# Performance work log

Measured on AMD Instinct MI355X. Metric: run time of the kernel, lower is better.

## Reference

```python
import jax, jax.numpy as jnp
import numpy as np

N_HEAD = 16
NEG = -1e30  # finite stand-in for -inf; keeps softmax NaN-free


def setup_inputs() -> dict:
    key = jax.random.key(0)
    k1, k2, k3, k4, k5, k6 = jax.random.split(key, 6)
    B, T, C = 4, 2048, 1024
    x = jax.random.normal(k1, (B, T, C), dtype=jnp.float32)
    # realistic right-padding: True = padded position
    lengths = jax.random.randint(k2, (B,), T // 2, T + 1)  # at least half valid
    padding_mask = jnp.arange(T)[None, :] >= lengths[:, None]  # [B,T] bool
    s = 0.02
    W_attn = jax.random.normal(k3, (C, 3 * C), dtype=jnp.float32) * s
    b_attn = jnp.zeros((3 * C,), dtype=jnp.float32)
    W_proj = jax.random.normal(k4, (C, C), dtype=jnp.float32) * s
    b_proj = jnp.zeros((C,), dtype=jnp.float32)
    return {"x": x, "padding_mask": padding_mask, "W_attn": W_attn,
            "b_attn": b_attn, "W_proj": W_proj, "b_proj": b_proj}


def reference(x, padding_mask, W_attn, b_attn, W_proj, b_proj):
    B, T, C = x.shape
    H, D = N_HEAD, C // N_HEAD
    qkv = x @ W_attn + b_attn  # [B,T,3C]
    q, k, v = jnp.split(qkv, 3, axis=-1)
    q = q.reshape(B, T, H, D).transpose(0, 2, 1, 3)  # [B,H,T,D]
    k = k.reshape(B, T, H, D).transpose(0, 2, 1, 3)
    v = v.reshape(B, T, H, D).transpose(0, 2, 1, 3)
    att = jnp.einsum('bhqd,bhkd->bhqk', q, k) / jnp.sqrt(jnp.float32(D))
    causal = jnp.tril(jnp.ones((T, T), dtype=bool))  # [T,T]
    invalid = padding_mask[:, None, None, :] | ~causal[None, None]  # [B,1,T,T] key invalid
    att = jnp.where(invalid, NEG, att)
    att = jax.nn.softmax(att, axis=-1)
    # rows where every key is masked: torch softmax gives NaN -> nan_to_num(0)
    any_valid = jnp.any(~invalid, axis=-1, keepdims=True)  # [B,1,T,1]
    att = jnp.where(any_valid, att, 0.0)
    y = jnp.einsum('bhqk,bhkd->bhqd', att, v)  # [B,H,T,D]
    y = y.transpose(0, 2, 1, 3).reshape(B, T, C)
    y = y @ W_proj + b_proj
    y = jnp.where(padding_mask[:, :, None], 0.0, y)
    return y
```

## Files before the change

kernel.cpp:

```cpp
#include <hip/hip_runtime.h>
#include <stdint.h>

#define T_SEQ 2048
#define CDIM  1024
#define NH    16
#define DH    64
#define BATCH 4
#define MROWS (BATCH * T_SEQ)
#define N3    (3 * CDIM)
#define NEGBIG -1e30f

typedef unsigned short u16;
typedef __attribute__((ext_vector_type(8))) __bf16 bf16x8;
typedef __attribute__((ext_vector_type(4))) __bf16 bf16x4;
typedef __attribute__((ext_vector_type(8))) unsigned short u16x8;
typedef __attribute__((ext_vector_type(4))) float f32x4;
typedef __attribute__((ext_vector_type(16))) float f32x16;
typedef __attribute__((ext_vector_type(4))) unsigned int u32x4;

__device__ inline u16 f2bf(float f) {
  uint32_t u = __builtin_bit_cast(uint32_t, f);
  u += 0x7FFFu + ((u >> 16) & 1u);
  return (u16)(u >> 16);
}

__device__ inline void gld_lds16(const void* g, void* l) {
  __builtin_amdgcn_global_load_lds(
      (const __attribute__((address_space(1))) void*)g,
      (__attribute__((address_space(3))) void*)l, 16, 0, 0);
}


__global__ __launch_bounds__(256) void cvt_f32_bf16(
    const float* __restrict__ in, u16* __restrict__ out, int n) {
  int i = (blockIdx.x * 256 + threadIdx.x) * 4;
  if (i >= n) return;
  float4 v = *(const float4*)&in[i];
  ushort4 o; o.x = f2bf(v.x); o.y = f2bf(v.y); o.z = f2bf(v.z); o.w = f2bf(v.w);
  *(ushort4*)&out[i] = o;
}

__global__ __launch_bounds__(256) void wt_tiled(
    const float* __restrict__ W, u16* __restrict__ WT, int K, int N) {
  __shared__ float tile[64][65];
  const int k0 = blockIdx.y * 64, n0 = blockIdx.x * 64;
  const int t = threadIdx.x, cr = t >> 6, cc = t & 63;
#pragma unroll
  for (int i = 0; i < 16; i++) {
    int r = i * 4 + cr;
    tile[r][cc] = W[(size_t)(k0 + r) * N + n0 + cc];
  }
  __syncthreads();
#pragma unroll
  for (int i = 0; i < 16; i++) {
    int r = i * 4 + cr;
    WT[(size_t)(n0 + r) * K + k0 + cc] = f2bf(tile[cc][r]);
  }
}

__global__ __launch_bounds__(256) void len_kernel(
    const void* __restrict__ maskp, int* __restrict__ lengths) {
  __shared__ int flag;
  __shared__ int red[256];
  const int t = threadIdx.x, b = blockIdx.x;
  if (t == 0) flag = 0;
  __syncthreads();
  const uint32_t* mw = (const uint32_t*)maskp;
  int f = 0;
  for (int i = t; i < 2048; i += 256) f |= (mw[i] > 1u) ? 1 : 0;
  if (f) atomicOr(&flag, 1);
  __syncthreads();
  int cnt = 0;
  if (flag) {
    const uint8_t* mb = (const uint8_t*)maskp;
    for (int i = t; i < T_SEQ; i += 256) cnt += (mb[(size_t)b * T_SEQ + i] == 0);
  } else {
    const int* mi = (const int*)maskp;
    for (int i = t; i < T_SEQ; i += 256) cnt += (mi[(size_t)b * T_SEQ + i] == 0);
  }
  red[t] = cnt;
  __syncthreads();
  for (int s = 128; s > 0; s >>= 1) {
    if (t < s) red[t] += red[t + s];
    __syncthreads();
  }
  if (t == 0) lengths[b] = red[0];
}

template <int MODE>
__global__ __launch_bounds__(256, 2) void gemm_bf16(
    const u16* __restrict__ A, const u16* __restrict__ Bt,
    const float* __restrict__ bias,
    u16* __restrict__ Qb, u16* __restrict__ Kb, u16* __restrict__ Vt,
    float* __restrict__ Out, const int* __restrict__ lengths,
    int Mdim, int Ndim, int Kdim) {
  __shared__ u16 SM[16384];
  u16* As = SM;
  u16* Bs = SM + 8192;
  const int t = threadIdx.x;
  const int lane = t & 63, wid = t >> 6;
  const int wr = wid >> 1, wc = wid & 1;
  const int r16 = lane & 15, kg = lane >> 4;
  const int m0 = blockIdx.y * 128, n0 = blockIdx.x * 128;

  f32x4 acc[4][4];
#pragma unroll
  for (int i = 0; i < 4; i++)
#pragma unroll
    for (int j = 0; j < 4; j++) acc[i][j] = (f32x4){0.f, 0.f, 0.f, 0.f};

  for (int k0 = 0; k0 < Kdim; k0 += 64) {
#pragma unroll
    for (int i = 0; i < 4; i++) {
      int idx = i * 256 + t;
      int row = idx >> 3;
      int chunk = idx & 7;
      int colel = (chunk * 8) ^ ((row & 7) << 3);
      gld_lds16(&A[(size_t)(m0 + row) * Kdim + k0 + colel], &As[idx * 8]);
      gld_lds16(&Bt[(size_t)(n0 + row) * Kdim + k0 + colel], &Bs[idx * 8]);
    }
    __syncthreads();

#pragma unroll
    for (int s = 0; s < 2; s++) {
      bf16x8 af[4], bfr[4];
#pragma unroll
      for (int m = 0; m < 4; m++) {
        int row = wr * 64 + m * 16 + r16;
        int colel = (s * 32 + kg * 8) ^ ((row & 7) << 3);
        af[m] = *(const bf16x8*)&As[row * 64 + colel];
      }
#pragma unroll
      for (int n = 0; n < 4; n++) {
        int row = wc * 64 + n * 16 + r16;
        int colel = (s * 32 + kg * 8) ^ ((row & 7) << 3);
        bfr[n] = *(const bf16x8*)&Bs[row * 64 + colel];
      }
#pragma unroll
      for (int m = 0; m < 4; m++)
#pragma unroll
        for (int n = 0; n < 4; n++)
          acc[m][n] = __builtin_amdgcn_mfma_f32_16x16x32_bf16(
              af[m], bfr[n], acc[m][n], 0, 0, 0);
    }
    __syncthreads();
  }

  if (MODE == 0 && n0 >= 2048) {
    u16* Tt = SM;
#pragma unroll
    for (int m = 0; m < 4; m++)
#pragma unroll
      for (int n = 0; n < 4; n++) {
        int ln = wc * 64 + n * 16 + r16;
        float bv = bias[n0 + ln];
#pragma unroll
        for (int reg = 0; reg < 4; reg++) {
          int lm = wr * 64 + m * 16 + kg * 4 + reg;
          Tt[ln * 128 + (lm ^ ((ln & 7) << 3))] = f2bf(acc[m][n][reg] + bv);
        }
      }
    __syncthreads();
    const int b = m0 >> 11;
    const int tt0 = m0 & 2047;
    const int cbase = n0 - 2048;
#pragma unroll
    for (int i = 0; i < 8; i++) {
      int u = i * 256 + t;
      int ln = u >> 4, ch = u & 15;
      u16x8 v = *(const u16x8*)&Tt[ln * 128 + ((ch * 8) ^ ((ln & 7) << 3))];
      int c = cbase + ln, hh = c >> 6, d = c & 63;
      *(u16x8*)&Vt[(((size_t)b * NH + hh) * DH + d) * T_SEQ + tt0 + ch * 8] = v;
    }
    return;
  }

#pragma unroll
  for (int m = 0; m < 4; m++) {
    int gmb = m0 + wr * 64 + m * 16 + kg * 4;
#pragma unroll
    for (int n = 0; n < 4; n++) {
      int gn = n0 + wc * 64 + n * 16 + r16;
      float bv = bias[gn];
#pragma unroll
      for (int reg = 0; reg < 4; reg++) {
        float v = acc[m][n][reg] + bv;
        int row = gmb + reg;
        int b = row >> 11, tt = row & 2047;
        if (MODE == 0) {
          int c = gn & 1023, h = c >> 6, d = c & 63;
          u16* dst = (gn < 1024) ? Qb : Kb;
          dst[((size_t)(b * NH + h) * T_SEQ + tt) * DH + d] = f2bf(v);
        } else {
          if (tt >= lengths[b]) v = 0.f;
          Out[(size_t)row * CDIM + gn] = v;
        }
      }
    }
  }
}

__global__ __launch_bounds__(256) void attn32p_kernel(
    const u16* __restrict__ Qb, const u16* __restrict__ Kb,
    const u16* __restrict__ Vt, u16* __restrict__ yb,
    const int* __restrict__ lengths) {
  __shared__ __attribute__((aligned(16))) char smem[32768];
  const int t = threadIdx.x, lane = t & 63, wid = t >> 6;
  const int l31 = lane & 31, hi = lane >> 5;
  const int wgid = blockIdx.x;
  const int xcd = wgid & 7, slot = wgid >> 3;
  const int bh = xcd * 8 + (slot >> 4);
  const int iq = slot & 15;
  const int b = bh >> 4, h = bh & (NH - 1);
  const int len = lengths[b];
  const int n64 = (len + 63) >> 6;
  const int npairs = (n64 + 1) >> 1;
  if (iq >= npairs) return;
  const int q0L = iq * 64;
  const int q0H = (n64 - 1 - iq) * 64;
  const bool hiAct = q0H > q0L;
  const int wp = wid >> 1, w2 = wid & 1;
  const bool act = (wp == 0) || hiAct;
  const int q0w = (wp ? q0H : q0L) + w2 * 32;
  const int qrow = q0w + l31;
  const u16* Qh = Qb + (size_t)bh * T_SEQ * DH;
  const u16* Kh = Kb + (size_t)bh * T_SEQ * DH;
  const u16* Vth = Vt + (size_t)bh * DH * T_SEQ;
  const float SC = 0.18033688011112042f;
  const float THR = 44.3614195558365f;

  const int kv_end = (hiAct ? q0H : q0L) + 64;
  const int ntiles = kv_end >> 6;

  bf16x8 qf[4];
#pragma unroll
  for (int ks = 0; ks < 4; ks++)
    qf[ks] = *(const bf16x8*)&Qh[(size_t)qrow * DH + ks * 16 + hi * 8];

  f32x16 oacc[2];
  oacc[0] = (f32x16)0.f; oacc[1] = (f32x16)0.f;
  float mrun = NEGBIG, lrun = 0.f;

  const int idx0 = t, idx1 = 256 + t;
  const int row0 = idx0 >> 3, ch0 = idx0 & 7;
  const int row1 = idx1 >> 3, ch1 = idx1 & 7;
  const int kc0 = (ch0 * 8) ^ ((row0 & 7) << 3);
  const int kc1 = (ch1 * 8) ^ ((row1 & 7) << 3);
  const char* kp0 = (const char*)Kh + ((size_t)row0 * DH + kc0) * 2;
  const char* kp1 = (const char*)Kh + ((size_t)row1 * DH + kc1) * 2;
  const char* vp0 = (const char*)Vth + ((size_t)row0 * T_SEQ + kc0) * 2;
  const char* vp1 = (const char*)Vth + ((size_t)row1 * T_SEQ + kc1) * 2;

  auto STAGE = [&](int bsel) {
    char* base = smem + bsel * 16384;
    gld_lds16(kp0, base + idx0 * 16);
    gld_lds16(kp1, base + idx1 * 16);
    gld_lds16(vp0, base + 8192 + idx0 * 16);
    gld_lds16(vp1, base + 8192 + idx1 * 16);
    kp0 += 8192; kp1 += 8192; vp0 += 128; vp1 += 128;
  };

  auto FLASH = [&](const u16* Ks, const u16* Vts, int kv0) {
    f32x16 sacc[2];
    sacc[0] = (f32x16)0.f; sacc[1] = (f32x16)0.f;
    __builtin_amdgcn_s_setprio(1);
#pragma unroll
    for (int kb = 0; kb < 2; kb++)
#pragma unroll
      for (int ks = 0; ks < 4; ks++) {
        int row = kb * 32 + l31;
        int col = (ks * 16 + hi * 8) ^ ((row & 7) << 3);
        bf16x8 ak = *(const bf16x8*)&Ks[row * 64 + col];
        sacc[kb] = __builtin_amdgcn_mfma_f32_32x32x16_bf16(
            ak, qf[ks], sacc[kb], 0, 0, 0);
      }
    __builtin_amdgcn_s_setprio(0);

    if ((kv0 + 63 > q0w) || (kv0 + 64 > len)) {
#pragma unroll
      for (int kb = 0; kb < 2; kb++)
#pragma unroll
        for (int r = 0; r < 16; r++) {
          int key = kv0 + kb * 32 + (r & 3) + 8 * (r >> 2) + 4 * hi;
          if (key > qrow || key >= len) sacc[kb][r] = NEGBIG;
        }
    }
    float tm[16];
#pragma unroll
    for (int r = 0; r < 16; r++) tm[r] = fmaxf(sacc[0][r], sacc[1][r]);
#pragma unroll
    for (int r = 0; r < 8; r++) tm[r] = fmaxf(tm[r], tm[r + 8]);
#pragma unroll
    for (int r = 0; r < 4; r++) tm[r] = fmaxf(tm[r], tm[r + 4]);
    tm[0] = fmaxf(fmaxf(tm[0], tm[2]), fmaxf(tm[1], tm[3]));
    float mt = fmaxf(tm[0], __shfl_xor(tm[0], 32));

    if (!__all(mt <= mrun + THR)) {
      float mnew = fmaxf(mrun, mt);
      float fac = exp2f((mrun - mnew) * SC);
      mrun = mnew;
      lrun *= fac;
#pragma unroll
      for (int r = 0; r < 16; r++) { oacc[0][r] *= fac; oacc[1][r] *= fac; }
    }
    const float msc = mrun * SC;
#pragma unroll
    for (int kb = 0; kb < 2; kb++)
#pragma unroll
      for (int r = 0; r < 16; r++)
        sacc[kb][r] = exp2f(fmaf(sacc[kb][r], SC, -msc));
    float pt[16];
#pragma unroll
    for (int r = 0; r < 16; r++) pt[r] = sacc[0][r] + sacc[1][r];
#pragma unroll
    for (int r = 0; r < 8; r++) pt[r] += pt[r + 8];
#pragma unroll
    for (int r = 0; r < 4; r++) pt[r] += pt[r + 4];
    float ps = (pt[0] + pt[2]) + (pt[1] + pt[3]);
    ps += __shfl_xor(ps, 32);
    lrun += ps;

#pragma unroll
    for (int ks = 0; ks < 4; ks++) {
      const int kb = ks >> 1, rb = (ks & 1) * 8;
      uint32_t d0, d1, d2, d3;
      asm("v_cvt_pk_bf16_f32 %0, %1, %2" : "=v"(d0)
          : "v"(sacc[kb][rb + 0]), "v"(sacc[kb][rb + 1]));
      asm("v_cvt_pk_bf16_f32 %0, %1, %2" : "=v"(d1)
          : "v"(sacc[kb][rb + 2]), "v"(sacc[kb][rb + 3]));
      asm("v_cvt_pk_bf16_f32 %0, %1, %2" : "=v"(d2)
          : "v"(sacc[kb][rb + 4]), "v"(sacc[kb][rb + 5]));
      asm("v_cvt_pk_bf16_f32 %0, %1, %2" : "=v"(d3)
          : "v"(sacc[kb][rb + 6]), "v"(sacc[kb][rb + 7]));
      bf16x8 pb = __builtin_bit_cast(bf16x8, (u32x4){d0, d1, d2, d3});
      __builtin_amdgcn_s_setprio(1);
#pragma unroll
      for (int mb = 0; mb < 2; mb++) {
        int row = mb * 32 + l31;
        int sw = (row & 7);
        bf16x4 v1 = *(const bf16x4*)&Vts[row * 64 + ((2 * ks) ^ sw) * 8 + 4 * hi];
        bf16x4 v2 = *(const bf16x4*)&Vts[row * 64 + ((2 * ks + 1) ^ sw) * 8 + 4 * hi];
        bf16x8 av;
#pragma unroll
        for (int j = 0; j < 4; j++) { av[j] = v1[j]; av[4 + j] = v2[j]; }
        oacc[mb] = __builtin_amdgcn_mfma_f32_32x32x16_bf16(
            av, pb, oacc[mb], 0, 0, 0);
      }
      __builtin_amdgcn_s_setprio(0);
    }
  };

  STAGE(0);
  for (int it = 0; it < ntiles; ++it) {
    asm volatile("s_waitcnt vmcnt(0)" ::: "memory");
    __builtin_amdgcn_s_barrier();
    __builtin_amdgcn_sched_barrier(0);
    if (it + 1 < ntiles) STAGE((it + 1) & 1);

    const u16* Ks  = (const u16*)(smem + (it & 1) * 16384);
    const u16* Vts = (const u16*)(smem + (it & 1) * 16384 + 8192);
    const int kv0 = it << 6;
    if (act && kv0 <= q0w + 31) FLASH(Ks, Vts, kv0);
  }
  __syncthreads();

  if (act) {
    u16* yt = (u16*)smem + wid * (32 * 72);
    const float inv = (lrun > 0.f) ? 1.f / lrun : 0.f;
#pragma unroll
    for (int mb = 0; mb < 2; mb++)
#pragma unroll
      for (int r = 0; r < 16; r += 2) {
        int d = mb * 32 + (r & 3) + 8 * (r >> 2) + 4 * hi;
        float a0 = oacc[mb][r] * inv, a1 = oacc[mb][r + 1] * inv;
        uint32_t pw;
        asm("v_cvt_pk_bf16_f32 %0, %1, %2" : "=v"(pw) : "v"(a0), "v"(a1));
        *(uint32_t*)&yt[l31 * 72 + d] = pw;
      }
    asm volatile("s_waitcnt lgkmcnt(0)" ::: "memory");
    __builtin_amdgcn_sched_barrier(0);
#pragma unroll
    for (int pass = 0; pass < 4; pass++) {
      int rowq = pass * 8 + (lane >> 3);
      int col8 = (lane & 7) * 8;
      u16x8 v = *(const u16x8*)&yt[rowq * 72 + col8];
      *(u16x8*)&yb[((size_t)b * T_SEQ + q0w + rowq) * CDIM + h * DH + col8] = v;
    }
  }
}

extern "C" void kernel_launch(void* const* d_in, const int* in_sizes, int n_in,
                              void* d_out, int out_size, void* d_ws, size_t ws_size,
                              hipStream_t stream) {
  const float* x  = (const float*)d_in[0];
  const void*  mask = d_in[1];
  const float* Wa = (const float*)d_in[2];
  const float* ba = (const float*)d_in[3];
  const float* Wp = (const float*)d_in[4];
  const float* bp = (const float*)d_in[5];
  float* out = (float*)d_out;

  char* w = (char*)d_ws;
  u16* xb  = (u16*)w; w += (size_t)MROWS * CDIM * 2;
  u16* WaT = (u16*)w; w += (size_t)N3 * CDIM * 2;
  u16* WpT = (u16*)w; w += (size_t)CDIM * CDIM * 2;
  u16* Qb  = (u16*)w; w += (size_t)MROWS * CDIM * 2;
  u16* Kb  = (u16*)w; w += (size_t)MROWS * CDIM * 2;
  u16* Vt  = (u16*)w; w += (size_t)MROWS * CDIM * 2;
  int* lengths = (int*)w;
  u16* yb = xb;

  cvt_f32_bf16<<<(MROWS * CDIM / 4 + 255) / 256, 256, 0, stream>>>(x, xb, MROWS * CDIM);
  wt_tiled<<<dim3(N3 / 64, CDIM / 64), 256, 0, stream>>>(Wa, WaT, CDIM, N3);
  wt_tiled<<<dim3(CDIM / 64, CDIM / 64), 256, 0, stream>>>(Wp, WpT, CDIM, CDIM);
  len_kernel<<<BATCH, 256, 0, stream>>>(mask, lengths);

  gemm_bf16<0><<<dim3(N3 / 128, MROWS / 128), 256, 0, stream>>>(
      xb, WaT, ba, Qb, Kb, Vt, nullptr, nullptr, MROWS, N3, CDIM);

  attn32p_kernel<<<dim3(1024), 256, 0, stream>>>(
      Qb, Kb, Vt, yb, lengths);

  gemm_bf16<1><<<dim3(CDIM / 128, MROWS / 128), 256, 0, stream>>>(
      yb, WpT, bp, nullptr, nullptr, nullptr, out, lengths, MROWS, CDIM, CDIM);
}
```

Before: 242.4 us.

## Load K/V fragments directly from global memory with permuted V layout

```diff
diff --git a/kernel.cpp b/kernel.cpp
--- a/kernel.cpp
+++ b/kernel.cpp
@@ -12,7 +12,6 @@
 
 typedef unsigned short u16;
 typedef __attribute__((ext_vector_type(8))) __bf16 bf16x8;
-typedef __attribute__((ext_vector_type(4))) __bf16 bf16x4;
 typedef __attribute__((ext_vector_type(8))) unsigned short u16x8;
 typedef __attribute__((ext_vector_type(4))) float f32x4;
 typedef __attribute__((ext_vector_type(16))) float f32x16;
@@ -170,7 +169,13 @@
       int ln = u >> 4, ch = u & 15;
       u16x8 v = *(const u16x8*)&Tt[ln * 128 + ((ch * 8) ^ ((ln & 7) << 3))];
       int c = cbase + ln, hh = c >> 6, d = c & 63;
-      *(u16x8*)&Vt[(((size_t)b * NH + hh) * DH + d) * T_SEQ + tt0 + ch * 8] = v;
+      size_t base = (((size_t)b * NH + hh) * DH + d) * T_SEQ;
+      int k0q = tt0 + ch * 8;
+      int shift = (ch & 1) << 2;
+      ushort4 qa; qa.x = (u16)v[0]; qa.y = (u16)v[1]; qa.z = (u16)v[2]; qa.w = (u16)v[3];
+      ushort4 qb; qb.x = (u16)v[4]; qb.y = (u16)v[5]; qb.z = (u16)v[6]; qb.w = (u16)v[7];
+      *(ushort4*)&Vt[base + k0q - shift] = qa;
+      *(ushort4*)&Vt[base + k0q + 8 - shift] = qb;
     }
     return;
   }
@@ -200,28 +205,22 @@
   }
 }
 
-__global__ __launch_bounds__(256) void attn32p_kernel(
+__global__ __launch_bounds__(256, 4) void attn32g_kernel(
     const u16* __restrict__ Qb, const u16* __restrict__ Kb,
     const u16* __restrict__ Vt, u16* __restrict__ yb,
     const int* __restrict__ lengths) {
-  __shared__ __attribute__((aligned(16))) char smem[32768];
+  __shared__ __attribute__((aligned(16))) u16 yts[4 * 32 * 72];
   const int t = threadIdx.x, lane = t & 63, wid = t >> 6;
   const int l31 = lane & 31, hi = lane >> 5;
   const int wgid = blockIdx.x;
   const int xcd = wgid & 7, slot = wgid >> 3;
   const int bh = xcd * 8 + (slot >> 4);
-  const int iq = slot & 15;
+  const int grp = slot & 15;
   const int b = bh >> 4, h = bh & (NH - 1);
   const int len = lengths[b];
-  const int n64 = (len + 63) >> 6;
-  const int npairs = (n64 + 1) >> 1;
-  if (iq >= npairs) return;
-  const int q0L = iq * 64;
-  const int q0H = (n64 - 1 - iq) * 64;
-  const bool hiAct = q0H > q0L;
-  const int wp = wid >> 1, w2 = wid & 1;
-  const bool act = (wp == 0) || hiAct;
-  const int q0w = (wp ? q0H : q0L) + w2 * 32;
+  if (grp * 128 >= len) return;
+  const int q0w = (grp * 4 + wid) * 32;
+  const bool act = q0w < len;
   const int qrow = q0w + l31;
   const u16* Qh = Qb + (size_t)bh * T_SEQ * DH;
   const u16* Kh = Kb + (size_t)bh * T_SEQ * DH;
@@ -229,143 +228,105 @@
   const float SC = 0.18033688011112042f;
   const float THR = 44.3614195558365f;
 
-  const int kv_end = (hiAct ? q0H : q0L) + 64;
-  const int ntiles = kv_end >> 6;
-
-  bf16x8 qf[4];
-#pragma unroll
-  for (int ks = 0; ks < 4; ks++)
-    qf[ks] = *(const bf16x8*)&Qh[(size_t)qrow * DH + ks * 16 + hi * 8];
-
-  f32x16 oacc[2];
-  oacc[0] = (f32x16)0.f; oacc[1] = (f32x16)0.f;
-  float mrun = NEGBIG, lrun = 0.f;
-
-  const int idx0 = t, idx1 = 256 + t;
-  const int row0 = idx0 >> 3, ch0 = idx0 & 7;
-  const int row1 = idx1 >> 3, ch1 = idx1 & 7;
-  const int kc0 = (ch0 * 8) ^ ((row0 & 7) << 3);
-  const int kc1 = (ch1 * 8) ^ ((row1 & 7) << 3);
-  const char* kp0 = (const char*)Kh + ((size_t)row0 * DH + kc0) * 2;
-  const char* kp1 = (const char*)Kh + ((size_t)row1 * DH + kc1) * 2;
-  const char* vp0 = (const char*)Vth + ((size_t)row0 * T_SEQ + kc0) * 2;
-  const char* vp1 = (const char*)Vth + ((size_t)row1 * T_SEQ + kc1) * 2;
-
-  auto STAGE = [&](int bsel) {
-    char* base = smem + bsel * 16384;
-    gld_lds16(kp0, base + idx0 * 16);
-    gld_lds16(kp1, base + idx1 * 16);
-    gld_lds16(vp0, base + 8192 + idx0 * 16);
-    gld_lds16(vp1, base + 8192 + idx1 * 16);
-    kp0 += 8192; kp1 += 8192; vp0 += 128; vp1 += 128;
-  };
-
-  auto FLASH = [&](const u16* Ks, const u16* Vts, int kv0) {
-    f32x16 sacc[2];
-    sacc[0] = (f32x16)0.f; sacc[1] = (f32x16)0.f;
-    __builtin_amdgcn_s_setprio(1);
-#pragma unroll
-    for (int kb = 0; kb < 2; kb++)
+  if (act) {
+    bf16x8 qf[4];
+#pragma unroll
+    for (int ks = 0; ks < 4; ks++)
+      qf[ks] = *(const bf16x8*)&Qh[(size_t)qrow * DH + ks * 16 + hi * 8];
+
+    f32x16 oacc[2];
+    oacc[0] = (f32x16)0.f; oacc[1] = (f32x16)0.f;
+    float mrun = NEGBIG, lrun = 0.f;
+
+    const int ntiles = (q0w >> 6) + 1;
+
+    for (int it = 0; it < ntiles; ++it) {
+      const int kv0 = it << 6;
+      const u16* Kt = Kh + (size_t)kv0 * DH;
+
+      f32x16 sacc[2];
+      sacc[0] = (f32x16)0.f; sacc[1] = (f32x16)0.f;
+      __builtin_amdgcn_s_setprio(1);
+#pragma unroll
+      for (int kb = 0; kb < 2; kb++)
+#pragma unroll
+        for (int ks = 0; ks < 4; ks++) {
+          bf16x8 ak = *(const bf16x8*)&Kt[(size_t)(kb * 32 + l31) * DH + ks * 16 + hi * 8];
+          sacc[kb] = __builtin_amdgcn_mfma_f32_32x32x16_bf16(
+              ak, qf[ks], sacc[kb], 0, 0, 0);
+        }
+      __builtin_amdgcn_s_setprio(0);
+
+      if ((kv0 + 63 > q0w) || (kv0 + 64 > len)) {
+#pragma unroll
+        for (int kb = 0; kb < 2; kb++)
+#pragma unroll
+          for (int r = 0; r < 16; r++) {
+            int key = kv0 + kb * 32 + (r & 3) + 8 * (r >> 2) + 4 * hi;
+            if (key > qrow || key >= len) sacc[kb][r] = NEGBIG;
+          }
+      }
+      float tm[16];
+#pragma unroll
+      for (int r = 0; r < 16; r++) tm[r] = fmaxf(sacc[0][r], sacc[1][r]);
+#pragma unroll
+      for (int r = 0; r < 8; r++) tm[r] = fmaxf(tm[r], tm[r + 8]);
+#pragma unroll
+      for (int r = 0; r < 4; r++) tm[r] = fmaxf(tm[r], tm[r + 4]);
+      tm[0] = fmaxf(fmaxf(tm[0], tm[2]), fmaxf(tm[1], tm[3]));
+      float mt = fmaxf(tm[0], __shfl_xor(tm[0], 32));
+
+      if (!__all(mt <= mrun + THR)) {
+        float mnew = fmaxf(mrun, mt);
+        float fac = exp2f((mrun - mnew) * SC);
+        mrun = mnew;
+        lrun *= fac;
+#pragma unroll
+        for (int r = 0; r < 16; r++) { oacc[0][r] *= fac; oacc[1][r] *= fac; }
+      }
+      const float msc = mrun * SC;
+#pragma unroll
+      for (int kb = 0; kb < 2; kb++)
+#pragma unroll
+        for (int r = 0; r < 16; r++)
+          sacc[kb][r] = exp2f(fmaf(sacc[kb][r], SC, -msc));
+      float pt[16];
+#pragma unroll
+      for (int r = 0; r < 16; r++) pt[r] = sacc[0][r] + sacc[1][r];
+#pragma unroll
+      for (int r = 0; r < 8; r++) pt[r] += pt[r + 8];
+#pragma unroll
+      for (int r = 0; r < 4; r++) pt[r] += pt[r + 4];
+      float ps = (pt[0] + pt[2]) + (pt[1] + pt[3]);
+      ps += __shfl_xor(ps, 32);
+      lrun += ps;
+
 #pragma unroll
       for (int ks = 0; ks < 4; ks++) {
-        int row = kb * 32 + l31;
-        int col = (ks * 16 + hi * 8) ^ ((row & 7) << 3);
-        bf16x8 ak = *(const bf16x8*)&Ks[row * 64 + col];
-        sacc[kb] = __builtin_amdgcn_mfma_f32_32x32x16_bf16(
-            ak, qf[ks], sacc[kb], 0, 0, 0);
-      }
-    __builtin_amdgcn_s_setprio(0);
-
-    if ((kv0 + 63 > q0w) || (kv0 + 64 > len)) {
-#pragma unroll
-      for (int kb = 0; kb < 2; kb++)
-#pragma unroll
-        for (int r = 0; r < 16; r++) {
-          int key = kv0 + kb * 32 + (r & 3) + 8 * (r >> 2) + 4 * hi;
-          if (key > qrow || key >= len) sacc[kb][r] = NEGBIG;
+        const int kb = ks >> 1, rb = (ks & 1) * 8;
+        uint32_t d0, d1, d2, d3;
+        asm("v_cvt_pk_bf16_f32 %0, %1, %2" : "=v"(d0)
+            : "v"(sacc[kb][rb + 0]), "v"(sacc[kb][rb + 1]));
+        asm("v_cvt_pk_bf16_f32 %0, %1, %2" : "=v"(d1)
+            : "v"(sacc[kb][rb + 2]), "v"(sacc[kb][rb + 3]));
+        asm("v_cvt_pk_bf16_f32 %0, %1, %2" : "=v"(d2)
+            : "v"(sacc[kb][rb + 4]), "v"(sacc[kb][rb + 5]));
+        asm("v_cvt_pk_bf16_f32 %0, %1, %2" : "=v"(d3)
+            : "v"(sacc[kb][rb + 6]), "v"(sacc[kb][rb + 7]));
+        bf16x8 pb = __builtin_bit_cast(bf16x8, (u32x4){d0, d1, d2, d3});
+        __builtin_amdgcn_s_setprio(1);
+#pragma unroll
+        for (int mb = 0; mb < 2; mb++) {
+          bf16x8 av = *(const bf16x8*)&Vth[(size_t)(mb * 32 + l31) * T_SEQ +
+                                           kv0 + ks * 16 + hi * 8];
+          oacc[mb] = __builtin_amdgcn_mfma_f32_32x32x16_bf16(
+              av, pb, oacc[mb], 0, 0, 0);
         }
-    }
-    float tm[16];
-#pragma unroll
-    for (int r = 0; r < 16; r++) tm[r] = fmaxf(sacc[0][r], sacc[1][r]);
-#pragma unroll
-    for (int r = 0; r < 8; r++) tm[r] = fmaxf(tm[r], tm[r + 8]);
-#pragma unroll
-    for (int r = 0; r < 4; r++) tm[r] = fmaxf(tm[r], tm[r + 4]);
-    tm[0] = fmaxf(fmaxf(tm[0], tm[2]), fmaxf(tm[1], tm[3]));
-    float mt = fmaxf(tm[0], __shfl_xor(tm[0], 32));
-
-    if (!__all(mt <= mrun + THR)) {
-      float mnew = fmaxf(mrun, mt);
-      float fac = exp2f((mrun - mnew) * SC);
-      mrun = mnew;
-      lrun *= fac;
-#pragma unroll
-      for (int r = 0; r < 16; r++) { oacc[0][r] *= fac; oacc[1][r] *= fac; }
-    }
-    const float msc = mrun * SC;
-#pragma unroll
-    for (int kb = 0; kb < 2; kb++)
-#pragma unroll
-      for (int r = 0; r < 16; r++)
-        sacc[kb][r] = exp2f(fmaf(sacc[kb][r], SC, -msc));
-    float pt[16];
-#pragma unroll
-    for (int r = 0; r < 16; r++) pt[r] = sacc[0][r] + sacc[1][r];
-#pragma unroll
-    for (int r = 0; r < 8; r++) pt[r] += pt[r + 8];
-#pragma unroll
-    for (int r = 0; r < 4; r++) pt[r] += pt[r + 4];
-    float ps = (pt[0] + pt[2]) + (pt[1] + pt[3]);
-    ps += __shfl_xor(ps, 32);
-    lrun += ps;
-
-#pragma unroll
-    for (int ks = 0; ks < 4; ks++) {
-      const int kb = ks >> 1, rb = (ks & 1) * 8;
-      uint32_t d0, d1, d2, d3;
-      asm("v_cvt_pk_bf16_f32 %0, %1, %2" : "=v"(d0)
-          : "v"(sacc[kb][rb + 0]), "v"(sacc[kb][rb + 1]));
-      asm("v_cvt_pk_bf16_f32 %0, %1, %2" : "=v"(d1)
-          : "v"(sacc[kb][rb + 2]), "v"(sacc[kb][rb + 3]));
-      asm("v_cvt_pk_bf16_f32 %0, %1, %2" : "=v"(d2)
-          : "v"(sacc[kb][rb + 4]), "v"(sacc[kb][rb + 5]));
-      asm("v_cvt_pk_bf16_f32 %0, %1, %2" : "=v"(d3)
-          : "v"(sacc[kb][rb + 6]), "v"(sacc[kb][rb + 7]));
-      bf16x8 pb = __builtin_bit_cast(bf16x8, (u32x4){d0, d1, d2, d3});
-      __builtin_amdgcn_s_setprio(1);
-#pragma unroll
-      for (int mb = 0; mb < 2; mb++) {
-        int row = mb * 32 + l31;
-        int sw = (row & 7);
-        bf16x4 v1 = *(const bf16x4*)&Vts[row * 64 + ((2 * ks) ^ sw) * 8 + 4 * hi];
-        bf16x4 v2 = *(const bf16x4*)&Vts[row * 64 + ((2 * ks + 1) ^ sw) * 8 + 4 * hi];
-        bf16x8 av;
-#pragma unroll
-        for (int j = 0; j < 4; j++) { av[j] = v1[j]; av[4 + j] = v2[j]; }
-        oacc[mb] = __builtin_amdgcn_mfma_f32_32x32x16_bf16(
-            av, pb, oacc[mb], 0, 0, 0);
-      }
-      __builtin_amdgcn_s_setprio(0);
-    }
-  };
-
-  STAGE(0);
-  for (int it = 0; it < ntiles; ++it) {
-    asm volatile("s_waitcnt vmcnt(0)" ::: "memory");
-    __builtin_amdgcn_s_barrier();
-    __builtin_amdgcn_sched_barrier(0);
-    if (it + 1 < ntiles) STAGE((it + 1) & 1);
-
-    const u16* Ks  = (const u16*)(smem + (it & 1) * 16384);
-    const u16* Vts = (const u16*)(smem + (it & 1) * 16384 + 8192);
-    const int kv0 = it << 6;
-    if (act && kv0 <= q0w + 31) FLASH(Ks, Vts, kv0);
-  }
-  __syncthreads();
-
-  if (act) {
-    u16* yt = (u16*)smem + wid * (32 * 72);
+        __builtin_amdgcn_s_setprio(0);
+      }
+    }
+
+    u16* yt = yts + wid * (32 * 72);
     const float inv = (lrun > 0.f) ? 1.f / lrun : 0.f;
 #pragma unroll
     for (int mb = 0; mb < 2; mb++)
@@ -418,7 +379,7 @@
   gemm_bf16<0><<<dim3(N3 / 128, MROWS / 128), 256, 0, stream>>>(
       xb, WaT, ba, Qb, Kb, Vt, nullptr, nullptr, MROWS, N3, CDIM);
 
-  attn32p_kernel<<<dim3(1024), 256, 0, stream>>>(
+  attn32g_kernel<<<dim3(1024), 256, 0, stream>>>(
       Qb, Kb, Vt, yb, lengths);
 
   gemm_bf16<1><<<dim3(CDIM / 128, MROWS / 128), 256, 0, stream>>>(
```

Result: slower. 345.9 us (+42.7%).
